# Kernel tuning notes

Hardware: AMD Instinct MI355X
Metric: run time of the kernel (lower is better)

The kernel has to match this reference:

```python
import jax, jax.numpy as jnp
import numpy as np

D_MODEL = 256
GEO_HIDDEN = 64
B, Q = 4, 1024


def setup_inputs() -> dict:
    key = jax.random.key(0)
    ks = jax.random.split(key, 10)
    q = jax.random.normal(ks[0], (B, Q, D_MODEL), dtype=jnp.float32)
    coords = jax.random.uniform(ks[1], (B, Q, 2), dtype=jnp.float32)
    active_mask = jax.random.bernoulli(ks[2], 0.7, (B, Q))
    W = jax.random.normal(ks[3], (D_MODEL, D_MODEL), dtype=jnp.float32) / jnp.sqrt(D_MODEL).astype(jnp.float32)
    # geo MLP params, stored [in, out] so forward is x @ w + b
    w1 = jax.random.normal(ks[4], (6, GEO_HIDDEN), dtype=jnp.float32) / jnp.sqrt(6.0).astype(jnp.float32)
    b1 = jnp.zeros((GEO_HIDDEN,), jnp.float32)
    w2 = jax.random.normal(ks[5], (GEO_HIDDEN, GEO_HIDDEN), dtype=jnp.float32) / jnp.sqrt(float(GEO_HIDDEN)).astype(jnp.float32)
    b2 = jnp.zeros((GEO_HIDDEN,), jnp.float32)
    w3 = jax.random.normal(ks[6], (GEO_HIDDEN, 1), dtype=jnp.float32) / jnp.sqrt(float(GEO_HIDDEN)).astype(jnp.float32)
    b3 = jnp.zeros((1,), jnp.float32)
    bias = jnp.zeros((1,), jnp.float32)
    return {"q": q, "coords": coords, "active_mask": active_mask,
            "W": W, "w1": w1, "b1": b1, "w2": w2, "b2": b2, "w3": w3, "b3": b3, "bias": bias}


def reference(q, coords, active_mask, W, w1, b1, w2, b2, w3, b3, bias):
    Bn, Qn, Dn = q.shape
    # bilinear query interaction: (q W) q^T -> [B,Q,Q]
    qW = q @ W
    bil = jnp.einsum("bqd,bkd->bqk", qW, q)

    # pairwise geometry features
    dx = coords[:, :, 0][:, :, None] - coords[:, :, 0][:, None, :]  # [B,Q,Q]
    dy = coords[:, :, 1][:, :, None] - coords[:, :, 1][:, None, :]
    dist2 = dx * dx + dy * dy
    dist = jnp.sqrt(dist2 + 1e-8)
    mask_zero = (jnp.abs(dx) < 1e-6) & (jnp.abs(dy) < 1e-6)
    dx_safe = jnp.where(mask_zero, 1e-6, dx)
    dy_safe = jnp.where(mask_zero, 1e-6, dy)
    ang = jnp.arctan2(dy_safe, dx_safe)
    geo = jnp.stack([dx, dy, dist, dist2, jnp.sin(ang), jnp.cos(ang)], axis=-1)  # [B,Q,Q,6]

    # tiny MLP 6 -> H -> H -> 1
    h = jax.nn.silu(geo @ w1 + b1)
    h = jax.nn.silu(h @ w2 + b2)
    geo_logits = (h @ w3 + b3)[..., 0]  # [B,Q,Q]

    logits = bil + geo_logits + bias
    # subtract diagonal (zero it out)
    eye = jnp.eye(Qn, dtype=bool)[None]
    logits = jnp.where(eye, 0.0, logits)
    # mask inactive pairs
    mm = active_mask[:, None, :] & active_mask[:, :, None]
    logits = jnp.where(mm, logits, -1e9)
    return logits
```

## Files before the change

kernel.cpp:

```cpp
#include <hip/hip_runtime.h>

typedef float f32x4 __attribute__((ext_vector_type(4)));
typedef __bf16 bf16x8 __attribute__((ext_vector_type(8)));

__device__ __forceinline__ unsigned short f2bf(float f) {
    union { float f; unsigned u; } v; v.f = f;
    return (unsigned short)((v.u + 0x8000u) >> 16);
}
__device__ __forceinline__ float hsilu(float x) {
    return x * __builtin_amdgcn_fmed3f(__builtin_fmaf(x, 0.25f, 0.5f), 0.f, 1.f);
}
__device__ __forceinline__ int sig_hid(int t) { return 16 * (t & 3) + (t >> 2); }

__global__ __launch_bounds__(256) void prep_kernel(
    const float* __restrict__ W, const float* __restrict__ w2,
    const float* __restrict__ w1, const float* __restrict__ b1,
    const int* __restrict__ amask, const float* __restrict__ coords,
    float* __restrict__ out, unsigned short* __restrict__ Wf,
    long long* __restrict__ w2f, long long* __restrict__ w1f,
    int* __restrict__ qlc, float2* __restrict__ ccomp, int* __restrict__ Na)
{
    const int blk = blockIdx.x, tid = threadIdx.x;

    if (blk < 1024) {
        const float4 v = make_float4(-1e9f, -1e9f, -1e9f, -1e9f);
        float4* o = (float4*)out + blk * 1024;
        o[tid] = v; o[256 + tid] = v; o[512 + tid] = v; o[768 + tid] = v;
        return;
    }
    if (blk < 1056) {
        int t = (blk - 1024) * 256 + tid;
        int f = t >> 6, lane = t & 63;
        int nt = f >> 3, s = f & 7;
        int quad = lane >> 4, l15 = lane & 15;
        unsigned short u[8];
        #pragma unroll
        for (int j = 0; j < 8; ++j)
            u[j] = f2bf(W[(32 * s + 8 * quad + j) * 256 + 16 * nt + l15]);
        *(uint4*)(Wf + t * 8) = *(const uint4*)u;
        return;
    }
    if (blk < 1058) {
        int t = (blk - 1056) * 256 + tid;
        int f = t >> 6, lane = t & 63;
        int n2 = f >> 1, s = f & 1;
        int quad = lane >> 4, l15 = lane & 15;
        int d[2];
        #pragma unroll
        for (int h = 0; h < 2; ++h) {
            float v[4];
            #pragma unroll
            for (int e = 0; e < 4; ++e) {
                int tp = 32 * s + 8 * quad + 4 * h + e;
                v[e] = w2[sig_hid(tp) * 64 + 16 * n2 + l15];
            }
            int lo = __builtin_amdgcn_cvt_pk_fp8_f32(v[0], v[1], 0, false);
            d[h]   = __builtin_amdgcn_cvt_pk_fp8_f32(v[2], v[3], lo, true);
        }
        long long pk; __builtin_memcpy(&pk, d, 8);
        w2f[t] = pk;
        return;
    }
    if (blk == 1058) {
        int n = tid >> 6, lane = tid & 63;
        int quad = lane >> 4, l15 = lane & 15;
        int col = 16 * n + l15;
        int d[2] = {0, 0};
        if (quad == 0) {
            float v0 = w1[0 * 64 + col], v1 = w1[1 * 64 + col];
            float v2 = w1[2 * 64 + col], v3 = w1[3 * 64 + col];
            float v4 = w1[4 * 64 + col], v5 = w1[5 * 64 + col];
            float v6 = b1[col];
            int lo = __builtin_amdgcn_cvt_pk_fp8_f32(v0, v1, 0, false);
            d[0]   = __builtin_amdgcn_cvt_pk_fp8_f32(v2, v3, lo, true);
            int l1 = __builtin_amdgcn_cvt_pk_fp8_f32(v4, v5, 0, false);
            d[1]   = __builtin_amdgcn_cvt_pk_fp8_f32(v6, 0.f, l1, true);
        }
        long long pk; __builtin_memcpy(&pk, d, 8);
        w1f[tid] = pk;
        return;
    }
    {
        __shared__ int ssum[256];
        int b = blk - 1059;
        const int* am = amask + b * 1024;
        const float2* cg = (const float2*)coords + b * 1024;
        int base = tid * 4;
        int m0 = am[base + 0] != 0, m1 = am[base + 1] != 0,
            m2 = am[base + 2] != 0, m3 = am[base + 3] != 0;
        int c = m0 + m1 + m2 + m3;
        ssum[tid] = c;
        __syncthreads();
        for (int off = 1; off < 256; off <<= 1) {
            int v = (tid >= off) ? ssum[tid - off] : 0;
            __syncthreads();
            ssum[tid] += v;
            __syncthreads();
        }
        int pos = ssum[tid] - c;
        int* ql = qlc + b * 1024;
        float2* cc = ccomp + b * 1024;
        if (m0) { ql[pos] = base + 0; cc[pos] = cg[base + 0]; pos++; }
        if (m1) { ql[pos] = base + 1; cc[pos] = cg[base + 1]; pos++; }
        if (m2) { ql[pos] = base + 2; cc[pos] = cg[base + 2]; pos++; }
        if (m3) { ql[pos] = base + 3; cc[pos] = cg[base + 3]; pos++; }
        if (tid == 255) Na[b] = ssum[255];
    }
}

__global__ __launch_bounds__(256) void qw_mfma_kernel(
    const float* __restrict__ q, const unsigned short* __restrict__ Wf,
    const int* __restrict__ qlc, const int* __restrict__ Na,
    unsigned short* __restrict__ qWc, unsigned short* __restrict__ qc)
{
    const int bb = blockIdx.y, iq = blockIdx.x;
    const int nb = Na[bb];
    if (iq * 16 >= nb) return;

    __shared__ unsigned char qs[16 * 512];
    const int tid = threadIdx.x;
    const int lane = tid & 63, wv = tid >> 6;
    const int l15 = lane & 15, quad = lane >> 4;

    #pragma unroll
    for (int it = 0; it < 4; ++it) {
        int s = tid + it * 256;
        int row = s >> 6, c64 = s & 63;
        int g = qlc[(bb << 10) + min(iq * 16 + row, nb - 1)];
        float4 v = ((const float4*)q)[(size_t)((bb << 10) + g) * 64 + c64];
        ushort4 u = make_ushort4(f2bf(v.x), f2bf(v.y), f2bf(v.z), f2bf(v.w));
        int off = row * 512 + (((c64 >> 1) ^ (row & 7)) << 4) + ((c64 & 1) << 3);
        *(ushort4*)(qs + off) = u;
        ((ushort4*)qc)[(size_t)((bb << 10) + iq * 16 + row) * 64 + c64] = u;
    }
    __syncthreads();

    bf16x8 a[8];
    #pragma unroll
    for (int s = 0; s < 8; ++s)
        a[s] = *(const bf16x8*)(qs + l15 * 512 + ((((s << 2) + quad) ^ (l15 & 7)) << 4));

    f32x4 acc[4];
    #pragma unroll
    for (int n = 0; n < 4; ++n) acc[n] = (f32x4){0.f, 0.f, 0.f, 0.f};
    const uint4* wf = (const uint4*)Wf;
    #pragma unroll
    for (int s = 0; s < 8; ++s) {
        #pragma unroll
        for (int n = 0; n < 4; ++n) {
            int nt = wv * 4 + n;
            uint4 braw = wf[(nt * 8 + s) * 64 + lane];
            acc[n] = __builtin_amdgcn_mfma_f32_16x16x32_bf16(
                a[s], __builtin_bit_cast(bf16x8, braw), acc[n], 0, 0, 0);
        }
    }
    #pragma unroll
    for (int n = 0; n < 4; ++n)
        #pragma unroll
        for (int r = 0; r < 4; ++r) {
            int row = iq * 16 + quad * 4 + r;
            int col = (wv * 4 + n) * 16 + l15;
            qWc[(size_t)((bb << 10) + row) * 256 + col] = f2bf(acc[n][r]);
        }
}

__global__ __launch_bounds__(256, 4) void edge_head_kernel(
    const unsigned short* __restrict__ qWc, const unsigned short* __restrict__ qc,
    const long long* __restrict__ w2f, const long long* __restrict__ w1f,
    const float2* __restrict__ ccomp,
    const int* __restrict__ qlc, const int* __restrict__ Na,
    const float* __restrict__ b2, const float* __restrict__ w3,
    const float* __restrict__ b3, const float* __restrict__ bias,
    float* __restrict__ out)
{
    __shared__ unsigned char qWs[16 * 512];
    __shared__ unsigned char qks[16 * 512];
    __shared__ __align__(16) unsigned char h1s[256 * 72];
    __shared__ float bilp[4 * 272];
    __shared__ float gs[256];

    const int tid  = threadIdx.x;
    const int lane = tid & 63;
    const int wv   = tid >> 6;
    const int l15  = lane & 15;
    const int quad = lane >> 4;

    long long w2frag[8], w1frag[4];
    #pragma unroll
    for (int f = 0; f < 8; ++f) w2frag[f] = w2f[f * 64 + lane];
    #pragma unroll
    for (int n = 0; n < 4; ++n) w1frag[n] = w1f[n * 64 + lane];
    float b2c[4], w3c[4];
    #pragma unroll
    for (int n = 0; n < 4; ++n) { b2c[n] = b2[16 * n + l15]; w3c[n] = w3[16 * n + l15]; }
    const float c0 = b3[0] + bias[0];

    int nt[4], off[5];
    off[0] = 0;
    #pragma unroll
    for (int b = 0; b < 4; ++b) {
        int nb = Na[b];
        nt[b] = (nb + 15) >> 4;
        off[b + 1] = off[b] + nt[b] * nt[b];
    }
    const int T = off[4];

    for (int t = blockIdx.x; t < T; t += gridDim.x) {
        int bb = 0;
        while (bb < 3 && t >= off[bb + 1]) bb++;
        int loc = t - off[bb];
        int ntb = nt[bb];
        int iq = loc / ntb, ik = loc - iq * ntb;
        int nb = Na[bb];

        {
            const uint4* qWg = (const uint4*)qWc + (size_t)((bb << 10) + iq * 16) * 32;
            const uint4* qkg = (const uint4*)qc  + (size_t)((bb << 10) + ik * 16) * 32;
            #pragma unroll
            for (int it = 0; it < 2; ++it) {
                int s = tid + it * 256;
                int row = s >> 5, c16 = s & 31;
                int o = row * 512 + ((c16 ^ (row & 7)) << 4);
                *(uint4*)(qWs + o) = qWg[s];
                *(uint4*)(qks + o) = qkg[s];
            }
            int qa = min(iq * 16 + (tid & 15), nb - 1);
            int ka = min(ik * 16 + (tid >> 4), nb - 1);
            float2 cq = ccomp[(bb << 10) + qa];
            float2 ck = ccomp[(bb << 10) + ka];
            float dx = cq.x - ck.x, dy = cq.y - ck.y;
            float dist2 = dx * dx + dy * dy;
            float dist = sqrtf(dist2 + 1e-8f);
            bool mz = (fabsf(dx) < 1e-6f) && (fabsf(dy) < 1e-6f);
            float dxs = mz ? 1e-6f : dx;
            float dys = mz ? 1e-6f : dy;
            float rinv = __builtin_amdgcn_rsqf(dxs * dxs + dys * dys);
            float sv = dys * rinv, cv = dxs * rinv;
            int a  = __builtin_amdgcn_cvt_pk_fp8_f32(dx, dy, 0, false);
            int d0 = __builtin_amdgcn_cvt_pk_fp8_f32(dist, dist2, a, true);
            int b  = __builtin_amdgcn_cvt_pk_fp8_f32(sv, cv, 0, false);
            int d1 = b | 0x00380000;
            *(int2*)(h1s + tid * 72 + 64) = make_int2(d0, d1);
        }
        __syncthreads();

        {
            f32x4 accb = {0.f, 0.f, 0.f, 0.f};
            #pragma unroll
            for (int i = 0; i < 2; ++i) {
                int s = 2 * wv + i;
                int o = l15 * 512 + ((((s << 2) + quad) ^ (l15 & 7)) << 4);
                bf16x8 av = *(const bf16x8*)(qWs + o);
                bf16x8 bv = *(const bf16x8*)(qks + o);
                accb = __builtin_amdgcn_mfma_f32_16x16x32_bf16(av, bv, accb, 0, 0, 0);
            }
            #pragma unroll
            for (int r = 0; r < 4; ++r)
                bilp[wv * 272 + (quad * 4 + r) * 17 + l15] = accb[r];
        }

        #pragma unroll
        for (int m = 0; m < 4; ++m) {
            int mt = wv * 4 + m;
            long long af = *(const long long*)(h1s + (mt * 16 + l15) * 72 + 64);
            f32x4 h[4];
            #pragma unroll
            for (int n = 0; n < 4; ++n)
                h[n] = __builtin_amdgcn_mfma_f32_16x16x32_fp8_fp8(
                    af, w1frag[n], (f32x4){0.f, 0.f, 0.f, 0.f}, 0, 0, 0);
            #pragma unroll
            for (int r = 0; r < 4; ++r) {
                float s0 = hsilu(h[0][r]), s1 = hsilu(h[1][r]);
                float s2 = hsilu(h[2][r]), s3 = hsilu(h[3][r]);
                int lo = __builtin_amdgcn_cvt_pk_fp8_f32(s0, s1, 0, false);
                int dw = __builtin_amdgcn_cvt_pk_fp8_f32(s2, s3, lo, true);
                *(int*)(h1s + (mt * 16 + quad * 4 + r) * 72 + l15 * 4) = dw;
            }
        }
        __syncthreads();

        #pragma unroll
        for (int tt = 0; tt < 4; ++tt) {
            int tm = wv * 4 + tt;
            unsigned rb = (unsigned)(tm * 16 + l15) * 72 + 8 * quad;
            long long a0 = *(const long long*)(h1s + rb);
            long long a1 = *(const long long*)(h1s + rb + 32);
            f32x4 acc[4];
            #pragma unroll
            for (int n = 0; n < 4; ++n)
                acc[n] = (f32x4){b2c[n], b2c[n], b2c[n], b2c[n]};
            #pragma unroll
            for (int n = 0; n < 4; ++n) {
                acc[n] = __builtin_amdgcn_mfma_f32_16x16x32_fp8_fp8(a0, w2frag[n * 2 + 0], acc[n], 0, 0, 0);
                acc[n] = __builtin_amdgcn_mfma_f32_16x16x32_fp8_fp8(a1, w2frag[n * 2 + 1], acc[n], 0, 0, 0);
            }
            float part[4] = {0.f, 0.f, 0.f, 0.f};
            #pragma unroll
            for (int n = 0; n < 4; ++n) {
                #pragma unroll
                for (int r = 0; r < 4; ++r)
                    part[r] = __builtin_fmaf(hsilu(acc[n][r]), w3c[n], part[r]);
            }
            #define SWZ_STEP(pat)                                                              \
                part[0] += __builtin_bit_cast(float, __builtin_amdgcn_ds_swizzle(__builtin_bit_cast(int, part[0]), pat)); \
                part[1] += __builtin_bit_cast(float, __builtin_amdgcn_ds_swizzle(__builtin_bit_cast(int, part[1]), pat)); \
                part[2] += __builtin_bit_cast(float, __builtin_amdgcn_ds_swizzle(__builtin_bit_cast(int, part[2]), pat)); \
                part[3] += __builtin_bit_cast(float, __builtin_amdgcn_ds_swizzle(__builtin_bit_cast(int, part[3]), pat));
            SWZ_STEP(0x041F)
            SWZ_STEP(0x081F)
            SWZ_STEP(0x101F)
            SWZ_STEP(0x201F)
            #undef SWZ_STEP
            float v01 = (l15 & 1) ? part[1] : part[0];
            float v23 = (l15 & 1) ? part[3] : part[2];
            float val = (l15 & 2) ? v23 : v01;
            if (l15 < 4)
                gs[tm * 16 + quad * 4 + l15] = val + c0;
        }
        __syncthreads();

        {
            int fq = tid >> 4, fk = tid & 15;
            float logit = bilp[0 * 272 + fq * 17 + fk] + bilp[1 * 272 + fq * 17 + fk]
                        + bilp[2 * 272 + fq * 17 + fk] + bilp[3 * 272 + fq * 17 + fk]
                        + gs[fk * 16 + fq];
            bool valid = (iq * 16 + fq < nb) && (ik * 16 + fk < nb);
            int qi = qlc[(bb << 10) + min(iq * 16 + fq, nb - 1)];
            int ki = qlc[(bb << 10) + min(ik * 16 + fk, nb - 1)];
            if (qi == ki) logit = 0.f;
            if (valid) out[(size_t)((bb << 10) + qi) * 1024 + ki] = logit;
        }
    }
}

extern "C" void kernel_launch(void* const* d_in, const int* in_sizes, int n_in,
                              void* d_out, int out_size, void* d_ws, size_t ws_size,
                              hipStream_t stream) {
    const float* q      = (const float*)d_in[0];
    const float* coords = (const float*)d_in[1];
    const int*   amask  = (const int*)d_in[2];
    const float* W      = (const float*)d_in[3];
    const float* w1     = (const float*)d_in[4];
    const float* b1     = (const float*)d_in[5];
    const float* w2     = (const float*)d_in[6];
    const float* b2     = (const float*)d_in[7];
    const float* w3     = (const float*)d_in[8];
    const float* b3     = (const float*)d_in[9];
    const float* bias   = (const float*)d_in[10];
    float* out = (float*)d_out;

    char* p = (char*)d_ws;
    unsigned short* qWc  = (unsigned short*)p;  p += 4096 * 256 * 2;
    unsigned short* qc   = (unsigned short*)p;  p += 4096 * 256 * 2;
    unsigned short* Wf   = (unsigned short*)p;  p += 8192 * 8 * 2;
    long long*      w2f  = (long long*)p;       p += 512 * 8;
    long long*      w1f  = (long long*)p;       p += 256 * 8;
    int*            qlc  = (int*)p;             p += 4096 * 4;
    float2*         ccomp= (float2*)p;          p += 4096 * 8;
    int*            Na   = (int*)p;

    prep_kernel<<<dim3(1063), dim3(256), 0, stream>>>(
        W, w2, w1, b1, amask, coords, out, Wf, w2f, w1f, qlc, ccomp, Na);
    qw_mfma_kernel<<<dim3(64, 4), dim3(256), 0, stream>>>(
        q, Wf, qlc, Na, qWc, qc);
    edge_head_kernel<<<dim3(1024), dim3(256), 0, stream>>>(
        qWc, qc, w2f, w1f, ccomp, qlc, Na, b2, w3, b3, bias, out);
}
```

Measured before the change: 130.5 us.

## Fuse qW projection into edge head kernel with contiguous tile ranges

Removes the separate qW MFMA kernel. The q-to-bf16 conversion moves into the prep kernel, and the edge kernel computes the 16-row qW tile on the fly whenever its query-row block changes. To make that reuse possible, tile assignment switches from grid-strided to a contiguous range per block, so consecutive tiles share the same iq. It also gathers key rows directly through the compacted index list, which saves one kernel launch and the qWc/qc round trip at the cost of recomputing qW tiles redundantly across blocks.

```diff
diff --git a/kernel.cpp b/kernel.cpp
--- a/kernel.cpp
+++ b/kernel.cpp
@@ -13,10 +13,12 @@
 __device__ __forceinline__ int sig_hid(int t) { return 16 * (t & 3) + (t >> 2); }
 
 __global__ __launch_bounds__(256) void prep_kernel(
+    const float* __restrict__ q,
     const float* __restrict__ W, const float* __restrict__ w2,
     const float* __restrict__ w1, const float* __restrict__ b1,
     const int* __restrict__ amask, const float* __restrict__ coords,
-    float* __restrict__ out, unsigned short* __restrict__ Wf,
+    float* __restrict__ out, unsigned short* __restrict__ qb16,
+    unsigned short* __restrict__ Wf,
     long long* __restrict__ w2f, long long* __restrict__ w1f,
     int* __restrict__ qlc, float2* __restrict__ ccomp, int* __restrict__ Na)
 {
@@ -26,6 +28,9 @@
         const float4 v = make_float4(-1e9f, -1e9f, -1e9f, -1e9f);
         float4* o = (float4*)out + blk * 1024;
         o[tid] = v; o[256 + tid] = v; o[512 + tid] = v; o[768 + tid] = v;
+        float4 qv = ((const float4*)q)[blk * 256 + tid];
+        ((ushort4*)qb16)[blk * 256 + tid] =
+            make_ushort4(f2bf(qv.x), f2bf(qv.y), f2bf(qv.z), f2bf(qv.w));
         return;
     }
     if (blk < 1056) {
@@ -84,7 +89,7 @@
         __shared__ int ssum[256];
         int b = blk - 1059;
         const int* am = amask + b * 1024;
-        const float2* cg = (const float2*)coords + b * 1024;
+        const float2* cg2 = (const float2*)coords + b * 1024;
         int base = tid * 4;
         int m0 = am[base + 0] != 0, m1 = am[base + 1] != 0,
             m2 = am[base + 2] != 0, m3 = am[base + 3] != 0;
@@ -100,72 +105,16 @@
         int pos = ssum[tid] - c;
         int* ql = qlc + b * 1024;
         float2* cc = ccomp + b * 1024;
-        if (m0) { ql[pos] = base + 0; cc[pos] = cg[base + 0]; pos++; }
-        if (m1) { ql[pos] = base + 1; cc[pos] = cg[base + 1]; pos++; }
-        if (m2) { ql[pos] = base + 2; cc[pos] = cg[base + 2]; pos++; }
-        if (m3) { ql[pos] = base + 3; cc[pos] = cg[base + 3]; pos++; }
+        if (m0) { ql[pos] = base + 0; cc[pos] = cg2[base + 0]; pos++; }
+        if (m1) { ql[pos] = base + 1; cc[pos] = cg2[base + 1]; pos++; }
+        if (m2) { ql[pos] = base + 2; cc[pos] = cg2[base + 2]; pos++; }
+        if (m3) { ql[pos] = base + 3; cc[pos] = cg2[base + 3]; pos++; }
         if (tid == 255) Na[b] = ssum[255];
     }
 }
 
-__global__ __launch_bounds__(256) void qw_mfma_kernel(
-    const float* __restrict__ q, const unsigned short* __restrict__ Wf,
-    const int* __restrict__ qlc, const int* __restrict__ Na,
-    unsigned short* __restrict__ qWc, unsigned short* __restrict__ qc)
-{
-    const int bb = blockIdx.y, iq = blockIdx.x;
-    const int nb = Na[bb];
-    if (iq * 16 >= nb) return;
-
-    __shared__ unsigned char qs[16 * 512];
-    const int tid = threadIdx.x;
-    const int lane = tid & 63, wv = tid >> 6;
-    const int l15 = lane & 15, quad = lane >> 4;
-
-    #pragma unroll
-    for (int it = 0; it < 4; ++it) {
-        int s = tid + it * 256;
-        int row = s >> 6, c64 = s & 63;
-        int g = qlc[(bb << 10) + min(iq * 16 + row, nb - 1)];
-        float4 v = ((const float4*)q)[(size_t)((bb << 10) + g) * 64 + c64];
-        ushort4 u = make_ushort4(f2bf(v.x), f2bf(v.y), f2bf(v.z), f2bf(v.w));
-        int off = row * 512 + (((c64 >> 1) ^ (row & 7)) << 4) + ((c64 & 1) << 3);
-        *(ushort4*)(qs + off) = u;
-        ((ushort4*)qc)[(size_t)((bb << 10) + iq * 16 + row) * 64 + c64] = u;
-    }
-    __syncthreads();
-
-    bf16x8 a[8];
-    #pragma unroll
-    for (int s = 0; s < 8; ++s)
-        a[s] = *(const bf16x8*)(qs + l15 * 512 + ((((s << 2) + quad) ^ (l15 & 7)) << 4));
-
-    f32x4 acc[4];
-    #pragma unroll
-    for (int n = 0; n < 4; ++n) acc[n] = (f32x4){0.f, 0.f, 0.f, 0.f};
-    const uint4* wf = (const uint4*)Wf;
-    #pragma unroll
-    for (int s = 0; s < 8; ++s) {
-        #pragma unroll
-        for (int n = 0; n < 4; ++n) {
-            int nt = wv * 4 + n;
-            uint4 braw = wf[(nt * 8 + s) * 64 + lane];
-            acc[n] = __builtin_amdgcn_mfma_f32_16x16x32_bf16(
-                a[s], __builtin_bit_cast(bf16x8, braw), acc[n], 0, 0, 0);
-        }
-    }
-    #pragma unroll
-    for (int n = 0; n < 4; ++n)
-        #pragma unroll
-        for (int r = 0; r < 4; ++r) {
-            int row = iq * 16 + quad * 4 + r;
-            int col = (wv * 4 + n) * 16 + l15;
-            qWc[(size_t)((bb << 10) + row) * 256 + col] = f2bf(acc[n][r]);
-        }
-}
-
 __global__ __launch_bounds__(256, 4) void edge_head_kernel(
-    const unsigned short* __restrict__ qWc, const unsigned short* __restrict__ qc,
+    const unsigned short* __restrict__ qb16, const unsigned short* __restrict__ Wf,
     const long long* __restrict__ w2f, const long long* __restrict__ w1f,
     const float2* __restrict__ ccomp,
     const int* __restrict__ qlc, const int* __restrict__ Na,
@@ -204,8 +153,13 @@
         off[b + 1] = off[b] + nt[b] * nt[b];
     }
     const int T = off[4];
-
-    for (int t = blockIdx.x; t < T; t += gridDim.x) {
+    const int len = (T + gridDim.x - 1) / gridDim.x;
+    const int t0 = blockIdx.x * len;
+    const int t1 = min(t0 + len, T);
+
+    int prev_key = -1;
+
+    for (int t = t0; t < t1; ++t) {
         int bb = 0;
         while (bb < 3 && t >= off[bb + 1]) bb++;
         int loc = t - off[bb];
@@ -213,16 +167,61 @@
         int iq = loc / ntb, ik = loc - iq * ntb;
         int nb = Na[bb];
 
+        int key = (bb << 8) | iq;
+        if (key != prev_key) {
+            prev_key = key;
+            #pragma unroll
+            for (int it = 0; it < 4; ++it) {
+                int s = tid + it * 256;
+                int row = s >> 6, c64 = s & 63;
+                int g = qlc[(bb << 10) + min(iq * 16 + row, nb - 1)];
+                ushort4 u = ((const ushort4*)qb16)[(size_t)((bb << 10) + g) * 64 + c64];
+                int o = row * 512 + (((c64 >> 1) ^ (row & 7)) << 4) + ((c64 & 1) << 3);
+                *(ushort4*)(qks + o) = u;
+            }
+            __syncthreads();
+
+            bf16x8 a[8];
+            #pragma unroll
+            for (int s = 0; s < 8; ++s)
+                a[s] = *(const bf16x8*)(qks + l15 * 512 + ((((s << 2) + quad) ^ (l15 & 7)) << 4));
+
+            f32x4 acc[4];
+            #pragma unroll
+            for (int n = 0; n < 4; ++n) acc[n] = (f32x4){0.f, 0.f, 0.f, 0.f};
+            const uint4* wf = (const uint4*)Wf;
+            #pragma unroll
+            for (int s = 0; s < 8; ++s) {
+                #pragma unroll
+                for (int n = 0; n < 4; ++n) {
+                    uint4 braw = wf[((wv * 4 + n) * 8 + s) * 64 + lane];
+                    acc[n] = __builtin_amdgcn_mfma_f32_16x16x32_bf16(
+                        a[s], __builtin_bit_cast(bf16x8, braw), acc[n], 0, 0, 0);
+                }
+            }
+            #pragma unroll
+            for (int n = 0; n < 4; ++n) {
+                #pragma unroll
+                for (int r = 0; r < 4; ++r) {
+                    int row = quad * 4 + r;
+                    int col = (wv * 4 + n) * 16 + l15;
+                    int c16 = col >> 3;
+                    int boff = row * 512 + ((c16 ^ (row & 7)) << 4) + (col & 7) * 2;
+                    *(unsigned short*)(qWs + boff) = f2bf(acc[n][r]);
+                }
+            }
+            __syncthreads();
+        }
+
         {
-            const uint4* qWg = (const uint4*)qWc + (size_t)((bb << 10) + iq * 16) * 32;
-            const uint4* qkg = (const uint4*)qc  + (size_t)((bb << 10) + ik * 16) * 32;
             #pragma unroll
             for (int it = 0; it < 2; ++it) {
                 int s = tid + it * 256;
                 int row = s >> 5, c16 = s & 31;
+                int g = qlc[(bb << 10) + min(ik * 16 + row, nb - 1)];
+                uint4 u = ((const uint4*)qb16)[(size_t)((bb << 10) + g) * 32 + c16];
                 int o = row * 512 + ((c16 ^ (row & 7)) << 4);
-                *(uint4*)(qWs + o) = qWg[s];
-                *(uint4*)(qks + o) = qkg[s];
+                *(uint4*)(qks + o) = u;
             }
             int qa = min(iq * 16 + (tid & 15), nb - 1);
             int ka = min(ik * 16 + (tid >> 4), nb - 1);
@@ -262,7 +261,8 @@
         #pragma unroll
         for (int m = 0; m < 4; ++m) {
             int mt = wv * 4 + m;
-            long long af = *(const long long*)(h1s + (mt * 16 + l15) * 72 + 64);
+            int2 fv = *(const int2*)(h1s + (mt * 16 + l15) * 72 + 64);
+            long long af = __builtin_bit_cast(long long, fv);
             f32x4 h[4];
             #pragma unroll
             for (int n = 0; n < 4; ++n)
@@ -283,8 +283,8 @@
         for (int tt = 0; tt < 4; ++tt) {
             int tm = wv * 4 + tt;
             unsigned rb = (unsigned)(tm * 16 + l15) * 72 + 8 * quad;
-            long long a0 = *(const long long*)(h1s + rb);
-            long long a1 = *(const long long*)(h1s + rb + 32);
+            long long a0 = __builtin_bit_cast(long long, *(const int2*)(h1s + rb));
+            long long a1 = __builtin_bit_cast(long long, *(const int2*)(h1s + rb + 32));
             f32x4 acc[4];
             #pragma unroll
             for (int n = 0; n < 4; ++n)
@@ -350,8 +350,7 @@
     float* out = (float*)d_out;
 
     char* p = (char*)d_ws;
-    unsigned short* qWc  = (unsigned short*)p;  p += 4096 * 256 * 2;
-    unsigned short* qc   = (unsigned short*)p;  p += 4096 * 256 * 2;
+    unsigned short* qb16 = (unsigned short*)p;  p += 4096 * 256 * 2;
     unsigned short* Wf   = (unsigned short*)p;  p += 8192 * 8 * 2;
     long long*      w2f  = (long long*)p;       p += 512 * 8;
     long long*      w1f  = (long long*)p;       p += 256 * 8;
@@ -360,9 +359,7 @@
     int*            Na   = (int*)p;
 
     prep_kernel<<<dim3(1063), dim3(256), 0, stream>>>(
-        W, w2, w1, b1, amask, coords, out, Wf, w2f, w1f, qlc, ccomp, Na);
-    qw_mfma_kernel<<<dim3(64, 4), dim3(256), 0, stream>>>(
-        q, Wf, qlc, Na, qWc, qc);
+        q, W, w2, w1, b1, amask, coords, out, qb16, Wf, w2f, w1f, qlc, ccomp, Na);
     edge_head_kernel<<<dim3(1024), dim3(256), 0, stream>>>(
-        qWc, qc, w2f, w1f, ccomp, qlc, Na, b2, w3, b3, bias, out);
-}
+        qb16, Wf, w2f, w1f, ccomp, qlc, Na, b2, w3, b3, bias, out);
+}
```

Result: slower. 170.9 us (+30.9%).
